# Performance work log

Hardware: AMD Instinct MI355X
Metric: run time of the kernel (lower is better)

Reference implementation:

```python
import jax, jax.numpy as jnp
import numpy as np

N_EVENTS = 16
N_SAMPLES = 2 ** 15          # 32768
STEP = 256                   # window_size // 2
LONG_WINDOW = 4096
LONG_COEFFS = LONG_WINDOW // 2 + 1   # 2049
LONG_STEP = LONG_WINDOW // 2         # 2048
LONG_FRAMES = N_SAMPLES // LONG_STEP # 16
N_FRAMES = N_SAMPLES // STEP         # 128
B = 8                                 # audio batch
BE = B * N_EVENTS                     # event batch = 128


def setup_inputs() -> dict:
    key = jax.random.key(0)
    k1, k2, k3, k4 = jax.random.split(key, 4)
    env = jax.random.uniform(k1, (BE, LONG_WINDOW, LONG_FRAMES), jnp.float32)
    tf = jax.random.normal(k2, (BE, LONG_COEFFS * 2, LONG_FRAMES), jnp.float32)
    noise = jax.random.uniform(k3, (BE, LONG_WINDOW, LONG_FRAMES), jnp.float32)
    indices = jax.random.randint(k4, (B, N_EVENTS), 0, N_FRAMES, dtype=jnp.int32)
    return {"env": env, "tf": tf, "noise": noise, "indices": indices}


def _event_render(env, tf, noise):
    # env, noise: (BE, LONG_WINDOW, LONG_FRAMES); tf: (BE, 2*LONG_COEFFS, LONG_FRAMES)
    batch = env.shape[0]
    energy = env * (noise * 2.0 - 1.0)  # uniform_(-1, 1) noise scaled by amp

    # magnitude = norm over interleaved (real, imag) pairs, per torch view semantics
    pairs = tf.reshape(batch, LONG_COEFFS, 2, LONG_FRAMES)
    mag = jnp.sqrt(jnp.sum(pairs * pairs, axis=2))  # (batch, C, F)
    mx = jnp.max(mag.reshape(batch, -1), axis=-1, keepdims=True)
    mag = (mag.reshape(batch, -1) / (mx + 1e-8)).reshape(batch, LONG_COEFFS, LONG_FRAMES)
    imag = tf[:, LONG_COEFFS:, :]
    phase = jnp.arctan2(imag, mag) * np.pi  # torch.angle(complex(mag, imag)) * pi
    tfc = mag * jnp.exp(1j * phase)         # complex transfer fn (batch, C, F)

    # sequential per-frame recurrence: state feeds through rfft/irfft filtering
    e_t = jnp.transpose(energy, (2, 0, 1))  # (F, batch, W)
    t_t = jnp.transpose(tfc, (2, 0, 1))     # (F, batch, C)

    def step(prev, inp):
        e, t = inp
        local = prev + e
        spec = jnp.fft.rfft(local, axis=-1, norm='ortho') * t
        frame = jnp.fft.irfft(spec, n=LONG_WINDOW, axis=-1, norm='ortho')
        return frame, frame

    init = jnp.zeros((batch, LONG_WINDOW), energy.dtype)
    _, frames = jax.lax.scan(step, init, (e_t, t_t))   # (F, batch, W)
    frames = jnp.transpose(frames, (1, 0, 2))          # (batch, F, W)

    # overlap-add with hop = LONG_STEP = W/2: split frames into halves and add
    halves = frames.reshape(batch, LONG_FRAMES, 2, LONG_STEP)
    out = jnp.zeros((batch, LONG_FRAMES + 1, LONG_STEP), frames.dtype)
    out = out.at[:, :LONG_FRAMES].add(halves[:, :, 0])
    out = out.at[:, 1:].add(halves[:, :, 1])
    return out.reshape(batch, -1)[:, :N_SAMPLES]       # (BE, N_SAMPLES)


def _segment_render(atoms, indices):
    # atoms: (BE, N_SAMPLES) -> (B, N_EVENTS, N_SAMPLES); scatter-add at time offsets
    x = atoms.reshape(B, N_EVENTS, N_SAMPLES)
    times = indices * STEP                                      # (B, E)
    pos = times[:, :, None] + jnp.arange(N_SAMPLES)[None, None, :]  # (B, E, S)
    out = jnp.zeros((B, 2 * N_SAMPLES), x.dtype)
    bidx = jnp.arange(B)[:, None, None]
    out = out.at[bidx, pos].add(x)
    return out[:, None, :N_SAMPLES]                             # (B, 1, N_SAMPLES)


def reference(env, tf, noise, indices):
    atoms = _event_render(env, tf, noise)
    return _segment_render(atoms, indices)
```

## Files before the change

### kernel.cpp

```cpp
#include <hip/hip_runtime.h>
#include <math.h>

#define TWO_PI 6.283185307179586f

#define OFF_ET   0ull
#define OFF_E    8388608ull
#define OFF_MAXP 16781312ull
#define OFF_Z    16782336ull

__device__ __forceinline__ int swz(int n) { return n ^ ((n >> 5) & 31); }

__device__ __forceinline__ int permf(int k) {
    return ((k & 1) << 10) | (((k >> 1) & 3) << 8) | (((k >> 3) & 3) << 6)
         | (((k >> 5) & 3) << 4) | (((k >> 7) & 3) << 2) | ((k >> 9) & 3);
}

__device__ __forceinline__ void r4_fwd(float* cr, float* ci, int j, int h, float ang) {
    int p0 = swz(j), p1 = swz(j + h), p2 = swz(j + 2 * h), p3 = swz(j + 3 * h);
    float ar = cr[p0], ai = ci[p0];
    float br = cr[p1], bi = ci[p1];
    float crr = cr[p2], cri = ci[p2];
    float drr = cr[p3], dri = ci[p3];
    float u0r = ar + crr, u0i = ai + cri;
    float u1r = ar - crr, u1i = ai - cri;
    float u2r = br + drr, u2i = bi + dri;
    float u3r = br - drr, u3i = bi - dri;
    float s1, c1; __sincosf(ang, &s1, &c1);
    float c2 = c1 * c1 - s1 * s1, s2 = 2.f * c1 * s1;
    float c3 = c1 * c2 - s1 * s2, s3 = s1 * c2 + c1 * s2;
    cr[p0] = u0r + u2r; ci[p0] = u0i + u2i;
    float z1r = u1r + u3i, z1i = u1i - u3r;
    cr[p1] = z1r * c1 + z1i * s1; ci[p1] = z1i * c1 - z1r * s1;
    float z2r = u0r - u2r, z2i = u0i - u2i;
    cr[p2] = z2r * c2 + z2i * s2; ci[p2] = z2i * c2 - z2r * s2;
    float z3r = u1r - u3i, z3i = u1i + u3r;
    cr[p3] = z3r * c3 + z3i * s3; ci[p3] = z3i * c3 - z3r * s3;
}

__device__ __forceinline__ void r4_inv(float* cr, float* ci, int j, int h, float ang) {
    int p0 = swz(j), p1 = swz(j + h), p2 = swz(j + 2 * h), p3 = swz(j + 3 * h);
    float z0r = cr[p0], z0i = ci[p0];
    float z1r = cr[p1], z1i = ci[p1];
    float z2r = cr[p2], z2i = ci[p2];
    float z3r = cr[p3], z3i = ci[p3];
    float s1, c1; __sincosf(ang, &s1, &c1);
    float c2 = c1 * c1 - s1 * s1, s2 = 2.f * c1 * s1;
    float c3 = c1 * c2 - s1 * s2, s3 = s1 * c2 + c1 * s2;
    float t1r = z1r * c1 - z1i * s1, t1i = z1i * c1 + z1r * s1;
    float t2r = z2r * c2 - z2i * s2, t2i = z2i * c2 + z2r * s2;
    float t3r = z3r * c3 - z3i * s3, t3i = z3i * c3 + z3r * s3;
    float u0r = z0r + t2r, u0i = z0i + t2i;
    float u1r = z0r - t2r, u1i = z0i - t2i;
    float u2r = t1r + t3r, u2i = t1i + t3i;
    float u3r = t1r - t3r, u3i = t1i - t3i;
    cr[p0] = u0r + u2r; ci[p0] = u0i + u2i;
    cr[p1] = u1r - u3i; ci[p1] = u1i + u3r;
    cr[p2] = u0r - u2r; ci[p2] = u0i - u2i;
    cr[p3] = u1r + u3i; ci[p3] = u1i - u3r;
}

__global__ __launch_bounds__(512) void k_fwd(const float* __restrict__ env,
                                             const float* __restrict__ noise,
                                             const float* __restrict__ tf,
                                             float* __restrict__ ws) {
    __shared__ float B[16384];
    int tid = threadIdx.x;
    int id = blockIdx.x;
    if (id < 512) {
        int xcd = id & 7, slot = id >> 3;
        int be = xcd * 16 + (slot >> 2);
        int fg = slot & 3;
        const float4* env4 = (const float4*)env;
        const float4* noi4 = (const float4*)noise;
        size_t base = (size_t)be * 16384 + fg;
        for (int it = 0; it < 8; ++it) {
            int n = it * 512 + tid;
            float4 e = env4[base + (size_t)n * 4];
            float4 z = noi4[base + (size_t)n * 4];
            float v0 = e.x * (z.x * 2.0f - 1.0f);
            float v1 = e.y * (z.y * 2.0f - 1.0f);
            float v2 = e.z * (z.z * 2.0f - 1.0f);
            float v3 = e.w * (z.w * 2.0f - 1.0f);
            int m = swz(n >> 1) + (n & 1) * 2048;
            B[m] = v0; B[4096 + m] = v1; B[8192 + m] = v2; B[12288 + m] = v3;
        }
        __syncthreads();
        for (int j = 0; j < 4; ++j) {
            float* cr = B + j * 4096;
            float* ci = cr + 2048;
#pragma unroll
            for (int it = 0; it < 2; ++it) {
                int i = tid + it * 512;
                int sj = swz(i), sjb = swz(i + 1024);
                float ar = cr[sj], ai = ci[sj], br = cr[sjb], bi = ci[sjb];
                float dr = ar - br, di = ai - bi;
                float s, c; __sincosf((float)i * (TWO_PI / 2048.0f), &s, &c);
                cr[sj] = ar + br; ci[sj] = ai + bi;
                cr[sjb] = dr * c + di * s; ci[sjb] = di * c - dr * s;
            }
            __syncthreads();
            r4_fwd(cr, ci, (tid >> 8) * 1024 + (tid & 255), 256, (float)(tid & 255) * (TWO_PI / 1024.0f)); __syncthreads();
            r4_fwd(cr, ci, (tid >> 6) * 256 + (tid & 63), 64, (float)(tid & 63) * (TWO_PI / 256.0f)); __syncthreads();
            r4_fwd(cr, ci, (tid & 31) * 64 + (tid >> 5), 16, (float)(tid >> 5) * (TWO_PI / 64.0f)); __syncthreads();
            r4_fwd(cr, ci, (tid & 127) * 16 + (tid >> 7), 4, (float)(tid >> 7) * (TWO_PI / 16.0f)); __syncthreads();
            r4_fwd(cr, ci, tid * 4, 1, 0.0f); __syncthreads();
            float2* Eg = (float2*)(ws + OFF_E) + (size_t)(be * 16 + fg * 4 + j) * 2049;
            for (int k = tid; k <= 1024; k += 512) {
                int pk = swz(permf(k));
                int pm = swz(permf((2048 - k) & 2047));
                float zkr = cr[pk], zki = ci[pk], zmr = cr[pm], zmi = ci[pm];
                float xer = 0.5f * (zkr + zmr), xei = 0.5f * (zki - zmi);
                float xor_ = 0.5f * (zki + zmi), xoi = 0.5f * (zmr - zkr);
                float s4, c4; __sincosf((float)k * (TWO_PI / 4096.0f), &s4, &c4);
                float wr = xor_ * c4 + xoi * s4;
                float wi = xoi * c4 - xor_ * s4;
                Eg[k] = make_float2(xer + wr, xei + wi);
                Eg[2048 - k] = make_float2(xer - wr, wi - xei);
            }
            __syncthreads();
        }
    } else {
        int bb = id - 512;
        int be = bb >> 1, c = bb & 1;
        const float4* ab4 = (const float4*)(tf + (size_t)be * 65568);
        float mx = 0.f;
        int start = c * 4098, end = start + 4098;
        for (int u = start + tid; u < end; u += 512) {
            int bin = u >> 2, e = u & 3;
            float4 A = ab4[bin * 8 + e];
            float4 Bv = ab4[bin * 8 + e + 4];
            mx = fmaxf(mx, fmaxf(fmaxf(A.x * A.x + Bv.x * Bv.x, A.y * A.y + Bv.y * Bv.y),
                                 fmaxf(A.z * A.z + Bv.z * Bv.z, A.w * A.w + Bv.w * Bv.w)));
        }
        B[tid] = mx;
        __syncthreads();
        for (int s = 256; s > 0; s >>= 1) {
            if (tid < s) B[tid] = fmaxf(B[tid], B[tid + s]);
            __syncthreads();
        }
        if (tid == 0) ws[OFF_MAXP + bb] = B[0];
    }
}

__global__ __launch_bounds__(256) void k_recur(const float* __restrict__ tf,
                                               float* __restrict__ ws) {
    __shared__ float sm2lo[256 * 17], simlo[256 * 17];
    __shared__ float sm2hi[256 * 17], simhi[256 * 17];
    int tid = threadIdx.x;
    int be = blockIdx.y;
    int k0 = blockIdx.x << 8;
    int hi0 = 1793 - k0;
    const float* tfb = tf + (size_t)be * 65568;
    const float4* ab4 = (const float4*)tfb;
    const float4* im4 = (const float4*)(tfb + 32784);

    for (int u = tid; u < 2048; u += 256) {
        int half = u >> 10, v = u & 1023;
        int g = v >> 2, e = v & 3;
        int bin = half ? (hi0 + g) : (k0 + g);
        float4 A = ab4[bin * 8 + e];
        float4 Bv = ab4[bin * 8 + e + 4];
        float4 I = im4[bin * 4 + e];
        int o = g * 17 + e * 4;
        float* sm = half ? sm2hi : sm2lo;
        float* si = half ? simhi : simlo;
        sm[o + 0] = A.x * A.x + Bv.x * Bv.x;
        sm[o + 1] = A.y * A.y + Bv.y * Bv.y;
        sm[o + 2] = A.z * A.z + Bv.z * Bv.z;
        sm[o + 3] = A.w * A.w + Bv.w * Bv.w;
        si[o + 0] = I.x; si[o + 1] = I.y; si[o + 2] = I.z; si[o + 3] = I.w;
    }
    __syncthreads();

    int k = k0 + tid;
    int m = 2048 - k;
    int rhi = 255 - tid;
    const float* mp = ws + OFF_MAXP + be * 2;
    float m2x = fmaxf(mp[0], mp[1]);
    float rden = 1.0f / (sqrtf(m2x) + 1e-8f);
    const float2* Eb = (const float2*)(ws + OFF_E) + (size_t)be * 16 * 2049;
    float2* Zb = (float2*)(ws + OFF_Z) + (size_t)be * 16 * 2048;
    float2 evlo[16], evhi[16];
#pragma unroll
    for (int f = 0; f < 16; ++f) {
        evlo[f] = Eb[(size_t)f * 2049 + k];
        evhi[f] = Eb[(size_t)f * 2049 + m];
    }
    float ym = (k == 0) ? 0.0f : 1.0f;
    float s4, c4; __sincosf((float)k * (TWO_PI / 4096.0f), &s4, &c4);
    const float SCL = 1.0f / 2048.0f;
    float srl = 0.f, sil = 0.f, srh = 0.f, sih = 0.f;
#pragma unroll
    for (int f = 0; f < 16; ++f) {
        float mh = sqrtf(sm2lo[tid * 17 + f]) * rden;
        float ph = atan2f(simlo[tid * 17 + f], mh) * 3.14159265358979f;
        float sp, cp; __sincosf(ph, &sp, &cp);
        float Tr = mh * cp, Ti = mh * sp;
        sil *= ym;
        srl += evlo[f].x; sil += evlo[f].y;
        float nr = srl * Tr - sil * Ti;
        sil = srl * Ti + sil * Tr; srl = nr;
        float mh2 = sqrtf(sm2hi[rhi * 17 + f]) * rden;
        float ph2 = atan2f(simhi[rhi * 17 + f], mh2) * 3.14159265358979f;
        float sp2, cp2; __sincosf(ph2, &sp2, &cp2);
        float Tr2 = mh2 * cp2, Ti2 = mh2 * sp2;
        sih *= ym;
        srh += evhi[f].x; sih += evhi[f].y;
        float nr2 = srh * Tr2 - sih * Ti2;
        sih = srh * Ti2 + sih * Tr2; srh = nr2;
        float2* Zf = Zb + (size_t)f * 2048;
        if (k == 0) {
            float y0 = srl * SCL, yn = srh * SCL;
            Zf[0] = make_float2(0.5f * (y0 + yn), 0.5f * (y0 - yn));
        } else {
            float ykr = srl * SCL, yki = sil * SCL;
            float ymr = srh * SCL, ymi = sih * SCL;
            float er = 0.5f * (ykr + ymr), ei = 0.5f * (yki - ymi);
            float dr = ykr - ymr, di = yki + ymi;
            float orr = 0.5f * (dr * c4 - di * s4);
            float oi = 0.5f * (dr * s4 + di * c4);
            Zf[k] = make_float2(er - oi, ei + orr);
            Zf[m] = make_float2(er + oi, orr - ei);
        }
    }
    if (k0 == 0 && tid == 0) {
        float sr = 0.f, si = 0.f;
#pragma unroll
        for (int f = 0; f < 16; ++f) {
            float a = tfb[1024 * 32 + f];
            float b = tfb[1024 * 32 + 16 + f];
            float im = tfb[32784 + 1024 * 16 + f];
            float mh = sqrtf(a * a + b * b) * rden;
            float ph = atan2f(im, mh) * 3.14159265358979f;
            float sp, cp; __sincosf(ph, &sp, &cp);
            float Tr = mh * cp, Ti = mh * sp;
            float2 e = Eb[(size_t)f * 2049 + 1024];
            sr += e.x; si += e.y;
            float nr = sr * Tr - si * Ti;
            si = sr * Ti + si * Tr; sr = nr;
            Zb[(size_t)f * 2048 + 1024] = make_float2(sr * SCL, -si * SCL);
        }
    }
}

__global__ __launch_bounds__(512) void k_fft_inv(float* __restrict__ ws) {
    __shared__ float cr[2048], ci[2048];
    int tid = threadIdx.x;
    int be = blockIdx.x >> 4, f = blockIdx.x & 15;
    const float4* Zg = (const float4*)((float2*)(ws + OFF_Z) + (size_t)(be * 16 + f) * 2048);
#pragma unroll
    for (int it = 0; it < 2; ++it) {
        int idx = tid + it * 512;
        float4 v = Zg[idx];
        int n0 = idx * 2;
        int p0 = swz(permf(n0)), p1 = swz(permf(n0 + 1));
        cr[p0] = v.x; ci[p0] = v.y;
        cr[p1] = v.z; ci[p1] = v.w;
    }
    __syncthreads();
    r4_inv(cr, ci, tid * 4, 1, 0.0f); __syncthreads();
    r4_inv(cr, ci, (tid & 127) * 16 + (tid >> 7), 4, (float)(tid >> 7) * (TWO_PI / 16.0f)); __syncthreads();
    r4_inv(cr, ci, (tid & 31) * 64 + (tid >> 5), 16, (float)(tid >> 5) * (TWO_PI / 64.0f)); __syncthreads();
    r4_inv(cr, ci, (tid >> 6) * 256 + (tid & 63), 64, (float)(tid & 63) * (TWO_PI / 256.0f)); __syncthreads();
    r4_inv(cr, ci, (tid >> 8) * 1024 + (tid & 255), 256, (float)(tid & 255) * (TWO_PI / 1024.0f)); __syncthreads();
#pragma unroll
    for (int it = 0; it < 2; ++it) {
        int i = tid + it * 512;
        int sj = swz(i), sjb = swz(i + 1024);
        float s, c; __sincosf((float)i * (TWO_PI / 2048.0f), &s, &c);
        float br = cr[sjb], bi = ci[sjb];
        float tr = br * c - bi * s, ti2 = br * s + bi * c;
        float ar = cr[sj], ai = ci[sj];
        cr[sj] = ar + tr;  ci[sj] = ai + ti2;
        cr[sjb] = ar - tr; ci[sjb] = ai - ti2;
    }
    __syncthreads();
    float2* Fg = (float2*)(ws + OFF_ET) + (size_t)(be * 16 + f) * 2048;
#pragma unroll
    for (int it = 0; it < 4; ++it) {
        int m = tid + it * 512;
        Fg[m] = make_float2(cr[swz(m)], ci[swz(m)]);
    }
}

__global__ __launch_bounds__(256) void k_segment(const float* __restrict__ ws,
                                                 const int* __restrict__ indices,
                                                 float* __restrict__ out) {
    __shared__ int ste[16];
    int tid = threadIdx.x;
    int b = blockIdx.y;
    if (tid < 16) ste[tid] = indices[b * 16 + tid] * 256;
    __syncthreads();
    int g = blockIdx.x * 256 + tid;
    int t = g << 2;
    const float* F = ws + OFF_ET;
    float4 acc = make_float4(0.f, 0.f, 0.f, 0.f);
#pragma unroll
    for (int e = 0; e < 16; ++e) {
        int te = ste[e];
        if (t >= te) {
            int d = t - te;
            int j = d >> 11, r = d & 2047;
            size_t base = (size_t)(b * 16 + e) * 65536;
            float4 v = *(const float4*)(F + base + j * 4096 + r);
            acc.x += v.x; acc.y += v.y; acc.z += v.z; acc.w += v.w;
            if (j >= 1) {
                float4 w = *(const float4*)(F + base + (j - 1) * 4096 + 2048 + r);
                acc.x += w.x; acc.y += w.y; acc.z += w.z; acc.w += w.w;
            }
        }
    }
    ((float4*)out)[(size_t)b * 8192 + g] = acc;
}

extern "C" void kernel_launch(void* const* d_in, const int* in_sizes, int n_in,
                              void* d_out, int out_size, void* d_ws, size_t ws_size,
                              hipStream_t stream) {
    const float* env = (const float*)d_in[0];
    const float* tf = (const float*)d_in[1];
    const float* noise = (const float*)d_in[2];
    const int* indices = (const int*)d_in[3];
    float* ws = (float*)d_ws;
    float* out = (float*)d_out;

    k_fwd<<<dim3(768), dim3(512), 0, stream>>>(env, noise, tf, ws);
    k_recur<<<dim3(4, 128), dim3(256), 0, stream>>>(tf, ws);
    k_fft_inv<<<dim3(2048), dim3(512), 0, stream>>>(ws);
    k_segment<<<dim3(32, 8), dim3(256), 0, stream>>>(ws, indices, out);
}
```

Measured before the change: 82.07 us.

## Batch four FFTs per block in forward and inverse kernels, sharing twiddles and barriers

The forward FFT kernel now runs all four frames' radix stages together, so each stage computes its twiddle once and issues one barrier instead of four. The inverse FFT kernel is reshaped the same way, with each block handling four frames in 64KB of shared memory, and its grid shrinks from 2048 to 512 blocks. This cuts sincos work and synchronisation, at the cost of more shared memory per block for the inverse kernel, fewer blocks, and possibly lower occupancy.

```diff
diff --git a/kernel.cpp b/kernel.cpp
--- a/kernel.cpp
+++ b/kernel.cpp
@@ -15,8 +15,8 @@
          | (((k >> 5) & 3) << 4) | (((k >> 7) & 3) << 2) | ((k >> 9) & 3);
 }
 
-__device__ __forceinline__ void r4_fwd(float* cr, float* ci, int j, int h, float ang) {
-    int p0 = swz(j), p1 = swz(j + h), p2 = swz(j + 2 * h), p3 = swz(j + 3 * h);
+__device__ __forceinline__ void r4f_core(float* cr, float* ci, int p0, int p1, int p2, int p3,
+                                         float c1, float s1, float c2, float s2, float c3, float s3) {
     float ar = cr[p0], ai = ci[p0];
     float br = cr[p1], bi = ci[p1];
     float crr = cr[p2], cri = ci[p2];
@@ -25,9 +25,6 @@
     float u1r = ar - crr, u1i = ai - cri;
     float u2r = br + drr, u2i = bi + dri;
     float u3r = br - drr, u3i = bi - dri;
-    float s1, c1; __sincosf(ang, &s1, &c1);
-    float c2 = c1 * c1 - s1 * s1, s2 = 2.f * c1 * s1;
-    float c3 = c1 * c2 - s1 * s2, s3 = s1 * c2 + c1 * s2;
     cr[p0] = u0r + u2r; ci[p0] = u0i + u2i;
     float z1r = u1r + u3i, z1i = u1i - u3r;
     cr[p1] = z1r * c1 + z1i * s1; ci[p1] = z1i * c1 - z1r * s1;
@@ -37,15 +34,12 @@
     cr[p3] = z3r * c3 + z3i * s3; ci[p3] = z3i * c3 - z3r * s3;
 }
 
-__device__ __forceinline__ void r4_inv(float* cr, float* ci, int j, int h, float ang) {
-    int p0 = swz(j), p1 = swz(j + h), p2 = swz(j + 2 * h), p3 = swz(j + 3 * h);
+__device__ __forceinline__ void r4i_core(float* cr, float* ci, int p0, int p1, int p2, int p3,
+                                         float c1, float s1, float c2, float s2, float c3, float s3) {
     float z0r = cr[p0], z0i = ci[p0];
     float z1r = cr[p1], z1i = ci[p1];
     float z2r = cr[p2], z2i = ci[p2];
     float z3r = cr[p3], z3i = ci[p3];
-    float s1, c1; __sincosf(ang, &s1, &c1);
-    float c2 = c1 * c1 - s1 * s1, s2 = 2.f * c1 * s1;
-    float c3 = c1 * c2 - s1 * s2, s3 = s1 * c2 + c1 * s2;
     float t1r = z1r * c1 - z1i * s1, t1i = z1i * c1 + z1r * s1;
     float t2r = z2r * c2 - z2i * s2, t2i = z2i * c2 + z2r * s2;
     float t3r = z3r * c3 - z3i * s3, t3i = z3i * c3 + z3r * s3;
@@ -59,10 +53,25 @@
     cr[p3] = u1r + u3i; ci[p3] = u1i - u3r;
 }
 
-__global__ __launch_bounds__(512) void k_fwd(const float* __restrict__ env,
-                                             const float* __restrict__ noise,
-                                             const float* __restrict__ tf,
-                                             float* __restrict__ ws) {
+#define STAGE4(CORE, JEXPR, H, ANG)                                            \
+    {                                                                          \
+        int j_ = (JEXPR);                                                      \
+        int p0 = swz(j_), p1 = swz(j_ + (H)), p2 = swz(j_ + 2 * (H)),          \
+            p3 = swz(j_ + 3 * (H));                                            \
+        float s1, c1; __sincosf((ANG), &s1, &c1);                              \
+        float c2 = c1 * c1 - s1 * s1, s2 = 2.f * c1 * s1;                      \
+        float c3 = c1 * c2 - s1 * s2, s3 = s1 * c2 + c1 * s2;                  \
+        CORE(B + 0,     B + 2048,  p0, p1, p2, p3, c1, s1, c2, s2, c3, s3);    \
+        CORE(B + 4096,  B + 6144,  p0, p1, p2, p3, c1, s1, c2, s2, c3, s3);    \
+        CORE(B + 8192,  B + 10240, p0, p1, p2, p3, c1, s1, c2, s2, c3, s3);    \
+        CORE(B + 12288, B + 14336, p0, p1, p2, p3, c1, s1, c2, s2, c3, s3);    \
+    }                                                                          \
+    __syncthreads();
+
+__global__ __launch_bounds__(512, 4) void k_fwd(const float* __restrict__ env,
+                                                const float* __restrict__ noise,
+                                                const float* __restrict__ tf,
+                                                float* __restrict__ ws) {
     __shared__ float B[16384];
     int tid = threadIdx.x;
     int id = blockIdx.x;
@@ -85,39 +94,48 @@
             B[m] = v0; B[4096 + m] = v1; B[8192 + m] = v2; B[12288 + m] = v3;
         }
         __syncthreads();
-        for (int j = 0; j < 4; ++j) {
-            float* cr = B + j * 4096;
-            float* ci = cr + 2048;
-#pragma unroll
-            for (int it = 0; it < 2; ++it) {
-                int i = tid + it * 512;
-                int sj = swz(i), sjb = swz(i + 1024);
+#pragma unroll
+        for (int it = 0; it < 2; ++it) {
+            int i = tid + it * 512;
+            int sj = swz(i), sjb = swz(i + 1024);
+            float s, c; __sincosf((float)i * (TWO_PI / 2048.0f), &s, &c);
+#pragma unroll
+            for (int j4 = 0; j4 < 4; ++j4) {
+                float* cr = B + j4 * 4096;
+                float* ci = cr + 2048;
                 float ar = cr[sj], ai = ci[sj], br = cr[sjb], bi = ci[sjb];
                 float dr = ar - br, di = ai - bi;
-                float s, c; __sincosf((float)i * (TWO_PI / 2048.0f), &s, &c);
                 cr[sj] = ar + br; ci[sj] = ai + bi;
                 cr[sjb] = dr * c + di * s; ci[sjb] = di * c - dr * s;
             }
-            __syncthreads();
-            r4_fwd(cr, ci, (tid >> 8) * 1024 + (tid & 255), 256, (float)(tid & 255) * (TWO_PI / 1024.0f)); __syncthreads();
-            r4_fwd(cr, ci, (tid >> 6) * 256 + (tid & 63), 64, (float)(tid & 63) * (TWO_PI / 256.0f)); __syncthreads();
-            r4_fwd(cr, ci, (tid & 31) * 64 + (tid >> 5), 16, (float)(tid >> 5) * (TWO_PI / 64.0f)); __syncthreads();
-            r4_fwd(cr, ci, (tid & 127) * 16 + (tid >> 7), 4, (float)(tid >> 7) * (TWO_PI / 16.0f)); __syncthreads();
-            r4_fwd(cr, ci, tid * 4, 1, 0.0f); __syncthreads();
-            float2* Eg = (float2*)(ws + OFF_E) + (size_t)(be * 16 + fg * 4 + j) * 2049;
-            for (int k = tid; k <= 1024; k += 512) {
+        }
+        __syncthreads();
+        STAGE4(r4f_core, (tid >> 8) * 1024 + (tid & 255), 256, (float)(tid & 255) * (TWO_PI / 1024.0f));
+        STAGE4(r4f_core, (tid >> 6) * 256 + (tid & 63), 64, (float)(tid & 63) * (TWO_PI / 256.0f));
+        STAGE4(r4f_core, (tid & 31) * 64 + (tid >> 5), 16, (float)(tid >> 5) * (TWO_PI / 64.0f));
+        STAGE4(r4f_core, (tid & 127) * 16 + (tid >> 7), 4, (float)(tid >> 7) * (TWO_PI / 16.0f));
+        STAGE4(r4f_core, tid * 4, 1, 0.0f);
+        float2* Ebase = (float2*)(ws + OFF_E) + (size_t)(be * 16 + fg * 4) * 2049;
+        for (int it = 0; it < 3; ++it) {
+            int k = tid + it * 512;
+            if (k <= 1024) {
                 int pk = swz(permf(k));
                 int pm = swz(permf((2048 - k) & 2047));
-                float zkr = cr[pk], zki = ci[pk], zmr = cr[pm], zmi = ci[pm];
-                float xer = 0.5f * (zkr + zmr), xei = 0.5f * (zki - zmi);
-                float xor_ = 0.5f * (zki + zmi), xoi = 0.5f * (zmr - zkr);
                 float s4, c4; __sincosf((float)k * (TWO_PI / 4096.0f), &s4, &c4);
-                float wr = xor_ * c4 + xoi * s4;
-                float wi = xoi * c4 - xor_ * s4;
-                Eg[k] = make_float2(xer + wr, xei + wi);
-                Eg[2048 - k] = make_float2(xer - wr, wi - xei);
+#pragma unroll
+                for (int j4 = 0; j4 < 4; ++j4) {
+                    float* cr = B + j4 * 4096;
+                    float* ci = cr + 2048;
+                    float zkr = cr[pk], zki = ci[pk], zmr = cr[pm], zmi = ci[pm];
+                    float xer = 0.5f * (zkr + zmr), xei = 0.5f * (zki - zmi);
+                    float xor_ = 0.5f * (zki + zmi), xoi = 0.5f * (zmr - zkr);
+                    float wr = xor_ * c4 + xoi * s4;
+                    float wi = xoi * c4 - xor_ * s4;
+                    float2* Eg = Ebase + (size_t)j4 * 2049;
+                    Eg[k] = make_float2(xer + wr, xei + wi);
+                    Eg[2048 - k] = make_float2(xer - wr, wi - xei);
+                }
             }
-            __syncthreads();
         }
     } else {
         int bb = id - 512;
@@ -243,43 +261,60 @@
     }
 }
 
-__global__ __launch_bounds__(512) void k_fft_inv(float* __restrict__ ws) {
-    __shared__ float cr[2048], ci[2048];
+__global__ __launch_bounds__(512, 4) void k_fft_inv(float* __restrict__ ws) {
+    __shared__ float B[16384];
     int tid = threadIdx.x;
-    int be = blockIdx.x >> 4, f = blockIdx.x & 15;
-    const float4* Zg = (const float4*)((float2*)(ws + OFF_Z) + (size_t)(be * 16 + f) * 2048);
-#pragma unroll
-    for (int it = 0; it < 2; ++it) {
-        int idx = tid + it * 512;
-        float4 v = Zg[idx];
-        int n0 = idx * 2;
-        int p0 = swz(permf(n0)), p1 = swz(permf(n0 + 1));
-        cr[p0] = v.x; ci[p0] = v.y;
-        cr[p1] = v.z; ci[p1] = v.w;
-    }
-    __syncthreads();
-    r4_inv(cr, ci, tid * 4, 1, 0.0f); __syncthreads();
-    r4_inv(cr, ci, (tid & 127) * 16 + (tid >> 7), 4, (float)(tid >> 7) * (TWO_PI / 16.0f)); __syncthreads();
-    r4_inv(cr, ci, (tid & 31) * 64 + (tid >> 5), 16, (float)(tid >> 5) * (TWO_PI / 64.0f)); __syncthreads();
-    r4_inv(cr, ci, (tid >> 6) * 256 + (tid & 63), 64, (float)(tid & 63) * (TWO_PI / 256.0f)); __syncthreads();
-    r4_inv(cr, ci, (tid >> 8) * 1024 + (tid & 255), 256, (float)(tid & 255) * (TWO_PI / 1024.0f)); __syncthreads();
+    int be = blockIdx.x >> 2, fg = blockIdx.x & 3;
+    const float2* Zbase = (const float2*)(ws + OFF_Z) + (size_t)(be * 16 + fg * 4) * 2048;
+#pragma unroll
+    for (int j4 = 0; j4 < 4; ++j4) {
+        const float4* Zg = (const float4*)(Zbase + (size_t)j4 * 2048);
+        float* cr = B + j4 * 4096;
+        float* ci = cr + 2048;
+#pragma unroll
+        for (int it = 0; it < 2; ++it) {
+            int idx = tid + it * 512;
+            float4 v = Zg[idx];
+            int n0 = idx * 2;
+            int p0 = swz(permf(n0)), p1 = swz(permf(n0 + 1));
+            cr[p0] = v.x; ci[p0] = v.y;
+            cr[p1] = v.z; ci[p1] = v.w;
+        }
+    }
+    __syncthreads();
+    STAGE4(r4i_core, tid * 4, 1, 0.0f);
+    STAGE4(r4i_core, (tid & 127) * 16 + (tid >> 7), 4, (float)(tid >> 7) * (TWO_PI / 16.0f));
+    STAGE4(r4i_core, (tid & 31) * 64 + (tid >> 5), 16, (float)(tid >> 5) * (TWO_PI / 64.0f));
+    STAGE4(r4i_core, (tid >> 6) * 256 + (tid & 63), 64, (float)(tid & 63) * (TWO_PI / 256.0f));
+    STAGE4(r4i_core, (tid >> 8) * 1024 + (tid & 255), 256, (float)(tid & 255) * (TWO_PI / 1024.0f));
 #pragma unroll
     for (int it = 0; it < 2; ++it) {
         int i = tid + it * 512;
         int sj = swz(i), sjb = swz(i + 1024);
         float s, c; __sincosf((float)i * (TWO_PI / 2048.0f), &s, &c);
-        float br = cr[sjb], bi = ci[sjb];
-        float tr = br * c - bi * s, ti2 = br * s + bi * c;
-        float ar = cr[sj], ai = ci[sj];
-        cr[sj] = ar + tr;  ci[sj] = ai + ti2;
-        cr[sjb] = ar - tr; ci[sjb] = ai - ti2;
-    }
-    __syncthreads();
-    float2* Fg = (float2*)(ws + OFF_ET) + (size_t)(be * 16 + f) * 2048;
-#pragma unroll
-    for (int it = 0; it < 4; ++it) {
-        int m = tid + it * 512;
-        Fg[m] = make_float2(cr[swz(m)], ci[swz(m)]);
+#pragma unroll
+        for (int j4 = 0; j4 < 4; ++j4) {
+            float* cr = B + j4 * 4096;
+            float* ci = cr + 2048;
+            float br = cr[sjb], bi = ci[sjb];
+            float tr = br * c - bi * s, ti2 = br * s + bi * c;
+            float ar = cr[sj], ai = ci[sj];
+            cr[sj] = ar + tr;  ci[sj] = ai + ti2;
+            cr[sjb] = ar - tr; ci[sjb] = ai - ti2;
+        }
+    }
+    __syncthreads();
+    float2* Fbase = (float2*)(ws + OFF_ET) + (size_t)(be * 16 + fg * 4) * 2048;
+#pragma unroll
+    for (int j4 = 0; j4 < 4; ++j4) {
+        float* cr = B + j4 * 4096;
+        float* ci = cr + 2048;
+        float2* Fg = Fbase + (size_t)j4 * 2048;
+#pragma unroll
+        for (int it = 0; it < 4; ++it) {
+            int m = tid + it * 512;
+            Fg[m] = make_float2(cr[swz(m)], ci[swz(m)]);
+        }
     }
 }
 
@@ -325,6 +360,6 @@
 
     k_fwd<<<dim3(768), dim3(512), 0, stream>>>(env, noise, tf, ws);
     k_recur<<<dim3(4, 128), dim3(256), 0, stream>>>(tf, ws);
-    k_fft_inv<<<dim3(2048), dim3(512), 0, stream>>>(ws);
+    k_fft_inv<<<dim3(512), dim3(512), 0, stream>>>(ws);
     k_segment<<<dim3(32, 8), dim3(256), 0, stream>>>(ws, indices, out);
 }
```

Result: no change. 83.15 us (+1.3%).
